# Optimization experiments

Hardware: AMD Instinct MI355X
Metric: run time of the kernel (lower is better)

## Reference

```python
import jax, jax.numpy as jnp
import numpy as np


def setup_inputs() -> dict:
    key = jax.random.key(0)
    k1, k2 = jax.random.split(key)
    B, N, D = 4, 2048, 1024
    context = jax.random.normal(k1, (B, N, D), dtype=jnp.float32)
    # Dense(embedding_dim*3): kernel [D, 3D], bias [3D] (glorot-ish scale)
    W_qkv = jax.random.normal(k2, (D, 3 * D), dtype=jnp.float32) * (1.0 / np.sqrt(D))
    b_qkv = jnp.zeros((3 * D,), dtype=jnp.float32)
    return {"context": context, "W_qkv": W_qkv, "b_qkv": b_qkv}


def reference(context, W_qkv, b_qkv):
    B, N, D = context.shape
    qkv = context @ W_qkv + b_qkv                       # [B, N, 3D]
    q, k, v = jnp.split(qkv, 3, axis=-1)                # each [B, N, D]
    scores = jnp.einsum("bnd,bmd->bnm", q, k)           # [B, N, N]
    # Faithful quirk: original divides by sqrt(scores.shape[-1]) == sqrt(N)
    scores = scores / jnp.asarray(np.sqrt(N), dtype=scores.dtype)
    causal = jnp.tril(jnp.ones((N, N), dtype=jnp.float32))  # lower-triangular
    scores = jnp.where(causal == 0, -jnp.inf, scores)
    probs = jax.nn.softmax(scores, axis=-1)             # [B, N, N]
    out = jnp.einsum("bnm,bmd->bnd", probs, v)          # [B, N, D]
    return out
```

## Files before the change

### kernel.cpp

```cpp
#include <hip/hip_runtime.h>
#include <cstdint>
#include <cstddef>


typedef __attribute__((ext_vector_type(8))) __bf16 bf16x8;
typedef __attribute__((ext_vector_type(4))) float f32x4;

__device__ inline unsigned short f2bf(float f) {
  unsigned u = __float_as_uint(f);
  u = (u + 0x7FFFu + ((u >> 16) & 1u)) >> 16;
  return (unsigned short)u;
}

__device__ inline void gld16(const void* g, void* l) {
  __builtin_amdgcn_global_load_lds(
      (const __attribute__((address_space(1))) unsigned int*)g,
      (__attribute__((address_space(3))) unsigned int*)l, 16, 0, 0);
}

template <bool SWAP>
__device__ inline void mma_mainloop(unsigned short* As, unsigned short* Bs,
                                    const unsigned short* Abase, long strideA,
                                    const unsigned short* Bbase, long strideB,
                                    int kIters, f32x4 acc[4][4]) {
  const int tid = threadIdx.x;
  const int lane = tid & 63;
  const int wave = tid >> 6;
  const int ry = (wave >> 1) * 64;
  const int rx = (wave & 1) * 64;
  const int lrow = lane >> 3;
  const int lcol = ((lane & 7) ^ lrow) * 8;

#pragma unroll
  for (int mi = 0; mi < 4; mi++)
#pragma unroll
    for (int nj = 0; nj < 4; nj++) acc[mi][nj] = (f32x4)(0.f);

  for (int kt = 0; kt < kIters; kt++) {
    const int k0 = kt * 64;
    __syncthreads();
#pragma unroll
    for (int c = 0; c < 4; c++) {
      const int q = wave * 4 + c;
      const int row = q * 8 + lrow;
      gld16(Abase + (size_t)row * strideA + k0 + lcol, &As[q * 512]);
      gld16(Bbase + (size_t)row * strideB + k0 + lcol, &Bs[q * 512]);
    }
    __syncthreads();
#pragma unroll
    for (int kk = 0; kk < 64; kk += 32) {
      const int cbase = (kk >> 3) + (lane >> 4);
      const int csw = ((cbase ^ (lane & 7)) << 3);
      bf16x8 a[4], b[4];
#pragma unroll
      for (int mi = 0; mi < 4; mi++)
        a[mi] = *(const bf16x8*)&As[(ry + mi * 16 + (lane & 15)) * 64 + csw];
#pragma unroll
      for (int nj = 0; nj < 4; nj++)
        b[nj] = *(const bf16x8*)&Bs[(rx + nj * 16 + (lane & 15)) * 64 + csw];
#pragma unroll
      for (int mi = 0; mi < 4; mi++)
#pragma unroll
        for (int nj = 0; nj < 4; nj++)
          acc[mi][nj] = SWAP
            ? __builtin_amdgcn_mfma_f32_16x16x32_bf16(b[nj], a[mi], acc[mi][nj], 0, 0, 0)
            : __builtin_amdgcn_mfma_f32_16x16x32_bf16(a[mi], b[nj], acc[mi][nj], 0, 0, 0);
    }
  }
}


__global__ void k_convert(const float* __restrict__ x, unsigned short* __restrict__ y, int n4) {
  int i = blockIdx.x * blockDim.x + threadIdx.x;
  if (i >= n4) return;
  float4 v = ((const float4*)x)[i];
  ushort4 o;
  o.x = f2bf(v.x); o.y = f2bf(v.y); o.z = f2bf(v.z); o.w = f2bf(v.w);
  ((ushort4*)y)[i] = o;
}

__global__ void k_transpose_w(const float* __restrict__ W, unsigned short* __restrict__ Wt) {
  __shared__ unsigned short sm[64 * 65];
  const int n0 = blockIdx.x * 64;
  const int k0 = blockIdx.y * 64;
  for (int i = threadIdx.x; i < 4096; i += 256) {
    int r = i >> 6, c = i & 63;
    sm[c * 65 + r] = f2bf(W[(size_t)(k0 + r) * 3072 + n0 + c]);
  }
  __syncthreads();
  for (int i = threadIdx.x; i < 4096; i += 256) {
    int r = i >> 6, c = i & 63;
    Wt[(size_t)(n0 + r) * 1024 + k0 + c] = sm[r * 65 + c];
  }
}


__global__ __launch_bounds__(256) void k_gemm_qkv(const unsigned short* __restrict__ A,
                                                  const unsigned short* __restrict__ Wt,
                                                  const float* __restrict__ bias,
                                                  unsigned short* __restrict__ qk,
                                                  unsigned short* __restrict__ vT) {
  __shared__ unsigned short As[128 * 64];
  __shared__ unsigned short Bs[128 * 64];
  f32x4 acc[4][4];
  const int tM0 = blockIdx.y * 128;
  const int lane = threadIdx.x & 63, wave = threadIdx.x >> 6;
  const int ry = (wave >> 1) * 64, rx = (wave & 1) * 64;
  const int l16 = lane & 15, rq = lane >> 4;

  if (blockIdx.x < 16) {
    const int tN0 = blockIdx.x * 128;
    mma_mainloop<true>(As, Bs, A + (size_t)tM0 * 1024, 1024,
                       Wt + (size_t)tN0 * 1024, 1024, 16, acc);
#pragma unroll
    for (int mi = 0; mi < 4; mi++) {
      const int m = tM0 + ry + mi * 16 + l16;
#pragma unroll
      for (int nj = 0; nj < 4; nj++) {
        const int n = tN0 + rx + nj * 16 + rq * 4;
        const float4 bv = *(const float4*)&bias[n];
        ushort4 o;
        o.x = f2bf(acc[mi][nj][0] + bv.x);
        o.y = f2bf(acc[mi][nj][1] + bv.y);
        o.z = f2bf(acc[mi][nj][2] + bv.z);
        o.w = f2bf(acc[mi][nj][3] + bv.w);
        *(ushort4*)&qk[(size_t)m * 2048 + n] = o;
      }
    }
  } else {
    const int tN0 = (blockIdx.x - 16) * 128;
    mma_mainloop<false>(As, Bs, A + (size_t)tM0 * 1024, 1024,
                        Wt + (size_t)(2048 + tN0) * 1024, 1024, 16, acc);
#pragma unroll
    for (int nj = 0; nj < 4; nj++) {
      const int d = tN0 + rx + nj * 16 + l16;
      const float bv = bias[2048 + d];
#pragma unroll
      for (int mi = 0; mi < 4; mi++) {
        const int m = tM0 + ry + mi * 16 + rq * 4;
        const int b = m >> 11, ns = m & 2047;
        ushort4 o;
        o.x = f2bf(acc[mi][nj][0] + bv);
        o.y = f2bf(acc[mi][nj][1] + bv);
        o.z = f2bf(acc[mi][nj][2] + bv);
        o.w = f2bf(acc[mi][nj][3] + bv);
        *(ushort4*)&vT[((size_t)(b * 1024 + d)) * 2048 + ns] = o;
      }
    }
  }
}

__global__ __launch_bounds__(256) void k_scores(const unsigned short* __restrict__ qk,
                                                unsigned short* __restrict__ P,
                                                float* __restrict__ l, float scale) {
  __shared__ unsigned short As[128 * 64];
  __shared__ unsigned short Bs[128 * 64];
  const int t = blockIdx.x, b = blockIdx.z;
  int qb = (int)((sqrtf(8.0f * (float)t + 1.0f) - 1.0f) * 0.5f);
  while (qb * (qb + 1) / 2 > t) qb--;
  while ((qb + 1) * (qb + 2) / 2 <= t) qb++;
  const int kb = t - qb * (qb + 1) / 2;
  f32x4 acc[4][4];
  const unsigned short* Aq = qk + ((size_t)(b * 2048 + qb * 128)) * 2048;
  const unsigned short* Bk = qk + ((size_t)(b * 2048 + kb * 128)) * 2048 + 1024;
  mma_mainloop<true>(As, Bs, Aq, 2048, Bk, 2048, 16, acc);
  const int lane = threadIdx.x & 63, wave = threadIdx.x >> 6;
  const int ry = (wave >> 1) * 64, rx = (wave & 1) * 64;
  const int l16 = lane & 15, rq = lane >> 4;
  unsigned short* Pb = P + ((size_t)(b * 2048 + qb * 128)) * 2048 + (size_t)kb * 128;
  float* lb = l + b * 2048 + qb * 128;
#pragma unroll
  for (int mi = 0; mi < 4; mi++) {
    const int m_local = ry + mi * 16 + l16;
    const int qi = qb * 128 + m_local;
    float rowpart = 0.f;
#pragma unroll
    for (int nj = 0; nj < 4; nj++) {
      const int n_base = rx + nj * 16 + rq * 4;
      ushort4 o;
      float p;
#pragma unroll
      for (int r = 0; r < 4; r++) {
        const int kj = kb * 128 + n_base + r;
        p = (kj <= qi) ? __expf(acc[mi][nj][r] * scale) : 0.f;
        rowpart += p;
        ((unsigned short*)&o)[r] = f2bf(p);
      }
      *(ushort4*)&Pb[(size_t)m_local * 2048 + n_base] = o;
    }
    rowpart += __shfl_xor(rowpart, 16, 64);
    rowpart += __shfl_xor(rowpart, 32, 64);
    if (rq == 0) atomicAdd(&lb[m_local], rowpart);
  }
}

__global__ __launch_bounds__(256) void k_pv(const unsigned short* __restrict__ P,
                                            const unsigned short* __restrict__ vT,
                                            const float* __restrict__ l,
                                            float* __restrict__ out) {
  __shared__ unsigned short As[128 * 64];
  __shared__ unsigned short Bs[128 * 64];
  const int db = blockIdx.x, b = blockIdx.z;
  int qb = blockIdx.y;
  if (b & 2) qb = 15 - qb;
  f32x4 acc[4][4];
  const unsigned short* Ap = P + ((size_t)(b * 2048 + qb * 128)) * 2048;
  const unsigned short* Bv = vT + ((size_t)(b * 1024 + db * 128)) * 2048;
  mma_mainloop<true>(As, Bs, Ap, 2048, Bv, 2048, (qb + 1) * 2, acc);
  const int lane = threadIdx.x & 63, wave = threadIdx.x >> 6;
  const int ry = (wave >> 1) * 64, rx = (wave & 1) * 64;
  const int l16 = lane & 15, rq = lane >> 4;
  const float* lb = l + b * 2048 + qb * 128;
  float* ob = out + ((size_t)(b * 2048 + qb * 128)) * 1024 + db * 128;
#pragma unroll
  for (int mi = 0; mi < 4; mi++) {
    const int m_local = ry + mi * 16 + l16;
    const float inv = 1.0f / lb[m_local];
#pragma unroll
    for (int nj = 0; nj < 4; nj++) {
      const int n_base = rx + nj * 16 + rq * 4;
      float4 o;
      o.x = acc[mi][nj][0] * inv;
      o.y = acc[mi][nj][1] * inv;
      o.z = acc[mi][nj][2] * inv;
      o.w = acc[mi][nj][3] * inv;
      *(float4*)&ob[(size_t)m_local * 1024 + n_base] = o;
    }
  }
}


extern "C" void kernel_launch(void* const* d_in, const int* in_sizes, int n_in,
                              void* d_out, int out_size, void* d_ws, size_t ws_size,
                              hipStream_t stream) {
  const float* ctx  = (const float*)d_in[0];
  const float* W    = (const float*)d_in[1];
  const float* bias = (const float*)d_in[2];
  float* out = (float*)d_out;

  char* ws = (char*)d_ws;
  unsigned short* Actx = (unsigned short*)(ws + 0);
  unsigned short* Wt   = (unsigned short*)(ws + 16777216);
  unsigned short* qk   = (unsigned short*)(ws + 23068672);
  unsigned short* vT   = (unsigned short*)(ws + 56623104);
  unsigned short* P    = (unsigned short*)(ws + 73400320);
  float*          lsum = (float*)(ws + 106954752);

  hipMemsetAsync(lsum, 0, 4 * 2048 * sizeof(float), stream);
  k_convert<<<8192, 256, 0, stream>>>(ctx, Actx, (8192 * 1024) / 4);
  k_transpose_w<<<dim3(48, 16), 256, 0, stream>>>(W, Wt);
  k_gemm_qkv<<<dim3(24, 64), 256, 0, stream>>>(Actx, Wt, bias, qk, vT);
  k_scores<<<dim3(136, 1, 4), 256, 0, stream>>>(qk, P, lsum, 0.022097086912079608f);
  k_pv<<<dim3(8, 16, 4), 256, 0, stream>>>(P, vT, lsum, out);
}
```

Measured before the change: 257.0 us.

## Double-buffer LDS tiles in scores and PV GEMMs; unify QKV mainloop

Adds a double-buffered mainloop that issues the global-to-LDS loads for the next K tile before computing on the current one, with a single barrier per iteration. The scores and PV kernels use it, so load latency can overlap with MFMA work. The QKV GEMM now always uses the swapped MFMA operand order. Its V-transpose epilogue changes to scalar 2-byte scattered stores in place of 8-byte vector stores. Shared memory per block doubles, which may lower occupancy. There is also a possible race: the next tile's async loads are only guarded by the single barrier before they are issued.

```diff
diff --git a/kernel.cpp b/kernel.cpp
--- a/kernel.cpp
+++ b/kernel.cpp
@@ -18,54 +18,84 @@
       (__attribute__((address_space(3))) unsigned int*)l, 16, 0, 0);
 }
 
-template <bool SWAP>
+__device__ inline void stage_tiles(unsigned short* As, unsigned short* Bs,
+                                   const unsigned short* Abase, long strideA,
+                                   const unsigned short* Bbase, long strideB,
+                                   int k0, int wave, int lrow, int lcol) {
+#pragma unroll
+  for (int c = 0; c < 4; c++) {
+    const int q = wave * 4 + c;
+    const int row = q * 8 + lrow;
+    gld16(Abase + (size_t)row * strideA + k0 + lcol, &As[q * 512]);
+    gld16(Bbase + (size_t)row * strideB + k0 + lcol, &Bs[q * 512]);
+  }
+}
+
+__device__ inline void compute_tiles(const unsigned short* As, const unsigned short* Bs,
+                                     int lane, int ry, int rx, f32x4 acc[4][4]) {
+#pragma unroll
+  for (int kk = 0; kk < 64; kk += 32) {
+    const int cbase = (kk >> 3) + (lane >> 4);
+    const int csw = ((cbase ^ (lane & 7)) << 3);
+    bf16x8 a[4], b[4];
+#pragma unroll
+    for (int mi = 0; mi < 4; mi++)
+      a[mi] = *(const bf16x8*)&As[(ry + mi * 16 + (lane & 15)) * 64 + csw];
+#pragma unroll
+    for (int nj = 0; nj < 4; nj++)
+      b[nj] = *(const bf16x8*)&Bs[(rx + nj * 16 + (lane & 15)) * 64 + csw];
+#pragma unroll
+    for (int mi = 0; mi < 4; mi++)
+#pragma unroll
+      for (int nj = 0; nj < 4; nj++)
+        acc[mi][nj] = __builtin_amdgcn_mfma_f32_16x16x32_bf16(b[nj], a[mi], acc[mi][nj], 0, 0, 0);
+  }
+}
+
 __device__ inline void mma_mainloop(unsigned short* As, unsigned short* Bs,
                                     const unsigned short* Abase, long strideA,
                                     const unsigned short* Bbase, long strideB,
                                     int kIters, f32x4 acc[4][4]) {
-  const int tid = threadIdx.x;
-  const int lane = tid & 63;
-  const int wave = tid >> 6;
-  const int ry = (wave >> 1) * 64;
-  const int rx = (wave & 1) * 64;
+  const int lane = threadIdx.x & 63, wave = threadIdx.x >> 6;
+  const int ry = (wave >> 1) * 64, rx = (wave & 1) * 64;
   const int lrow = lane >> 3;
   const int lcol = ((lane & 7) ^ lrow) * 8;
-
 #pragma unroll
   for (int mi = 0; mi < 4; mi++)
 #pragma unroll
     for (int nj = 0; nj < 4; nj++) acc[mi][nj] = (f32x4)(0.f);
-
   for (int kt = 0; kt < kIters; kt++) {
-    const int k0 = kt * 64;
     __syncthreads();
-#pragma unroll
-    for (int c = 0; c < 4; c++) {
-      const int q = wave * 4 + c;
-      const int row = q * 8 + lrow;
-      gld16(Abase + (size_t)row * strideA + k0 + lcol, &As[q * 512]);
-      gld16(Bbase + (size_t)row * strideB + k0 + lcol, &Bs[q * 512]);
-    }
+    stage_tiles(As, Bs, Abase, strideA, Bbase, strideB, kt * 64, wave, lrow, lcol);
     __syncthreads();
-#pragma unroll
-    for (int kk = 0; kk < 64; kk += 32) {
-      const int cbase = (kk >> 3) + (lane >> 4);
-      const int csw = ((cbase ^ (lane & 7)) << 3);
-      bf16x8 a[4], b[4];
-#pragma unroll
-      for (int mi = 0; mi < 4; mi++)
-        a[mi] = *(const bf16x8*)&As[(ry + mi * 16 + (lane & 15)) * 64 + csw];
-#pragma unroll
-      for (int nj = 0; nj < 4; nj++)
-        b[nj] = *(const bf16x8*)&Bs[(rx + nj * 16 + (lane & 15)) * 64 + csw];
-#pragma unroll
-      for (int mi = 0; mi < 4; mi++)
-#pragma unroll
-        for (int nj = 0; nj < 4; nj++)
-          acc[mi][nj] = SWAP
-            ? __builtin_amdgcn_mfma_f32_16x16x32_bf16(b[nj], a[mi], acc[mi][nj], 0, 0, 0)
-            : __builtin_amdgcn_mfma_f32_16x16x32_bf16(a[mi], b[nj], acc[mi][nj], 0, 0, 0);
-    }
+    compute_tiles(As, Bs, lane, ry, rx, acc);
+  }
+}
+
+__device__ inline void mma_mainloop_db(unsigned short* As0, unsigned short* Bs0,
+                                       unsigned short* As1, unsigned short* Bs1,
+                                       const unsigned short* Abase, long strideA,
+                                       const unsigned short* Bbase, long strideB,
+                                       int kIters, f32x4 acc[4][4]) {
+  const int lane = threadIdx.x & 63, wave = threadIdx.x >> 6;
+  const int ry = (wave >> 1) * 64, rx = (wave & 1) * 64;
+  const int lrow = lane >> 3;
+  const int lcol = ((lane & 7) ^ lrow) * 8;
+#pragma unroll
+  for (int mi = 0; mi < 4; mi++)
+#pragma unroll
+    for (int nj = 0; nj < 4; nj++) acc[mi][nj] = (f32x4)(0.f);
+  stage_tiles(As0, Bs0, Abase, strideA, Bbase, strideB, 0, wave, lrow, lcol);
+  for (int kt = 0; kt < kIters; kt++) {
+    __syncthreads();
+    unsigned short* Asc = (kt & 1) ? As1 : As0;
+    unsigned short* Bsc = (kt & 1) ? Bs1 : Bs0;
+    if (kt + 1 < kIters) {
+      unsigned short* Asn = (kt & 1) ? As0 : As1;
+      unsigned short* Bsn = (kt & 1) ? Bs0 : Bs1;
+      stage_tiles(Asn, Bsn, Abase, strideA, Bbase, strideB, (kt + 1) * 64, wave, lrow, lcol);
+    }
+    compute_tiles(Asc, Bsc, lane, ry, rx, acc);
   }
 }
 
@@ -107,11 +137,13 @@
   const int lane = threadIdx.x & 63, wave = threadIdx.x >> 6;
   const int ry = (wave >> 1) * 64, rx = (wave & 1) * 64;
   const int l16 = lane & 15, rq = lane >> 4;
-
-  if (blockIdx.x < 16) {
-    const int tN0 = blockIdx.x * 128;
-    mma_mainloop<true>(As, Bs, A + (size_t)tM0 * 1024, 1024,
-                       Wt + (size_t)tN0 * 1024, 1024, 16, acc);
+  const bool isQK = blockIdx.x < 16;
+  const int tN0 = isQK ? blockIdx.x * 128 : (blockIdx.x - 16) * 128;
+  const unsigned short* Wtile = Wt + (size_t)(isQK ? tN0 : 2048 + tN0) * 1024;
+
+  mma_mainloop(As, Bs, A + (size_t)tM0 * 1024, 1024, Wtile, 1024, 16, acc);
+
+  if (isQK) {
 #pragma unroll
     for (int mi = 0; mi < 4; mi++) {
       const int m = tM0 + ry + mi * 16 + l16;
@@ -128,23 +160,17 @@
       }
     }
   } else {
-    const int tN0 = (blockIdx.x - 16) * 128;
-    mma_mainloop<false>(As, Bs, A + (size_t)tM0 * 1024, 1024,
-                        Wt + (size_t)(2048 + tN0) * 1024, 1024, 16, acc);
-#pragma unroll
-    for (int nj = 0; nj < 4; nj++) {
-      const int d = tN0 + rx + nj * 16 + l16;
-      const float bv = bias[2048 + d];
-#pragma unroll
-      for (int mi = 0; mi < 4; mi++) {
-        const int m = tM0 + ry + mi * 16 + rq * 4;
-        const int b = m >> 11, ns = m & 2047;
-        ushort4 o;
-        o.x = f2bf(acc[mi][nj][0] + bv);
-        o.y = f2bf(acc[mi][nj][1] + bv);
-        o.z = f2bf(acc[mi][nj][2] + bv);
-        o.w = f2bf(acc[mi][nj][3] + bv);
-        *(ushort4*)&vT[((size_t)(b * 1024 + d)) * 2048 + ns] = o;
+#pragma unroll
+    for (int mi = 0; mi < 4; mi++) {
+      const int m = tM0 + ry + mi * 16 + l16;
+      const int b = m >> 11, ns = m & 2047;
+#pragma unroll
+      for (int nj = 0; nj < 4; nj++) {
+        const int d0 = tN0 + rx + nj * 16 + rq * 4;
+        const float4 bv = *(const float4*)&bias[2048 + d0];
+#pragma unroll
+        for (int r = 0; r < 4; r++)
+          vT[((size_t)(b * 1024 + d0 + r)) * 2048 + ns] = f2bf(acc[mi][nj][r] + ((const float*)&bv)[r]);
       }
     }
   }
@@ -153,8 +179,8 @@
 __global__ __launch_bounds__(256) void k_scores(const unsigned short* __restrict__ qk,
                                                 unsigned short* __restrict__ P,
                                                 float* __restrict__ l, float scale) {
-  __shared__ unsigned short As[128 * 64];
-  __shared__ unsigned short Bs[128 * 64];
+  __shared__ unsigned short As0[128 * 64], Bs0[128 * 64];
+  __shared__ unsigned short As1[128 * 64], Bs1[128 * 64];
   const int t = blockIdx.x, b = blockIdx.z;
   int qb = (int)((sqrtf(8.0f * (float)t + 1.0f) - 1.0f) * 0.5f);
   while (qb * (qb + 1) / 2 > t) qb--;
@@ -163,7 +189,7 @@
   f32x4 acc[4][4];
   const unsigned short* Aq = qk + ((size_t)(b * 2048 + qb * 128)) * 2048;
   const unsigned short* Bk = qk + ((size_t)(b * 2048 + kb * 128)) * 2048 + 1024;
-  mma_mainloop<true>(As, Bs, Aq, 2048, Bk, 2048, 16, acc);
+  mma_mainloop_db(As0, Bs0, As1, Bs1, Aq, 2048, Bk, 2048, 16, acc);
   const int lane = threadIdx.x & 63, wave = threadIdx.x >> 6;
   const int ry = (wave >> 1) * 64, rx = (wave & 1) * 64;
   const int l16 = lane & 15, rq = lane >> 4;
@@ -198,15 +224,15 @@
                                             const unsigned short* __restrict__ vT,
                                             const float* __restrict__ l,
                                             float* __restrict__ out) {
-  __shared__ unsigned short As[128 * 64];
-  __shared__ unsigned short Bs[128 * 64];
+  __shared__ unsigned short As0[128 * 64], Bs0[128 * 64];
+  __shared__ unsigned short As1[128 * 64], Bs1[128 * 64];
   const int db = blockIdx.x, b = blockIdx.z;
   int qb = blockIdx.y;
   if (b & 2) qb = 15 - qb;
   f32x4 acc[4][4];
   const unsigned short* Ap = P + ((size_t)(b * 2048 + qb * 128)) * 2048;
   const unsigned short* Bv = vT + ((size_t)(b * 1024 + db * 128)) * 2048;
-  mma_mainloop<true>(As, Bs, Ap, 2048, Bv, 2048, (qb + 1) * 2, acc);
+  mma_mainloop_db(As0, Bs0, As1, Bs1, Ap, 2048, Bv, 2048, (qb + 1) * 2, acc);
   const int lane = threadIdx.x & 63, wave = threadIdx.x >> 6;
   const int ry = (wave >> 1) * 64, rx = (wave & 1) * 64;
   const int l16 = lane & 15, rq = lane >> 4;
```

Result: slower. 284.4 us (+10.7%).
